# Kernel tuning notes

Hardware: AMD Instinct MI355X
Metric: run time of the kernel (lower is better)

## Reference

```python
import jax, jax.numpy as jnp
import numpy as np

N_NODES = 50000


def _gcn_norm(edge_index, num_nodes):
    # PyG GCNConv default: add self-loops, symmetric normalization D^-1/2 A D^-1/2
    src, dst = edge_index[0], edge_index[1]
    loops = jnp.arange(num_nodes, dtype=src.dtype)
    src = jnp.concatenate([src, loops])
    dst = jnp.concatenate([dst, loops])
    deg = jax.ops.segment_sum(jnp.ones_like(src, dtype=jnp.float32), dst,
                              num_segments=num_nodes)
    dis = jnp.where(deg > 0, jax.lax.rsqrt(jnp.maximum(deg, 1.0)), 0.0)
    norm = dis[src] * dis[dst]  # [E']
    return src, dst, norm


def _gcn_conv(x, W, b, src, dst, norm, num_nodes):
    h = x @ W                                   # [N, out] transform first
    msg = h[src] * norm[:, None]                # [E', out] gather + scale
    agg = jax.ops.segment_sum(msg, dst, num_segments=num_nodes)  # scatter-add
    return agg + b


def setup_inputs() -> dict:
    key = jax.random.key(0)
    k1, k2, k3, k4 = jax.random.split(key, 4)
    n, e, d_in, d_h = N_NODES, 800000, 256, 128
    basic_block = jax.random.normal(k1, (n, d_in), dtype=jnp.float32)
    edge_index = jax.random.randint(k2, (2, e), 0, n, dtype=jnp.int64)
    W1 = jax.random.normal(k3, (d_in, d_h), dtype=jnp.float32) * (1.0 / np.sqrt(d_in))
    b1 = jnp.zeros((d_h,), dtype=jnp.float32)
    W2 = jax.random.normal(k4, (d_h, d_h), dtype=jnp.float32) * (1.0 / np.sqrt(d_h))
    b2 = jnp.zeros((d_h,), dtype=jnp.float32)
    return {"basic_block": basic_block, "edge_index": edge_index,
            "W1": W1, "b1": b1, "W2": W2, "b2": b2}


def reference(basic_block, edge_index, W1, b1, W2, b2):
    n = basic_block.shape[0]
    src, dst, norm = _gcn_norm(edge_index, n)
    x = jax.nn.relu(_gcn_conv(basic_block, W1, b1, src, dst, norm, n))
    x = _gcn_conv(x, W2, b2, src, dst, norm, n)
    return x
```

## Files before the change

### kernel.cpp

```cpp
#include <hip/hip_runtime.h>
#include <hip/hip_bf16.h>
#include <stdint.h>

#define D_H 128

typedef __bf16 bf16_t;
typedef unsigned short u16;
typedef bf16_t bf16x8 __attribute__((ext_vector_type(8)));
typedef bf16_t bf16x4 __attribute__((ext_vector_type(4)));
typedef float  f32x4  __attribute__((ext_vector_type(4)));

__global__ void k_pre(const int* __restrict__ dst, int* __restrict__ cnt4,
                      u16* __restrict__ rank, int E, int Nn, int gcr,
                      const float* __restrict__ W1, bf16_t* __restrict__ W1h,
                      bf16_t* __restrict__ W1l, int K1,
                      const float* __restrict__ W2, bf16_t* __restrict__ W2h,
                      bf16_t* __restrict__ W2l, int K2) {
    int bx = (int)blockIdx.x;
    if (bx < gcr) {
        int e = bx * 256 + threadIdx.x;
        if (e < E) {
            int d = dst[e];
            rank[e] = (u16)atomicAdd(&cnt4[(bx & 3) * Nn + d], 1);
        }
        return;
    }
    int id = (bx - gcr) * 256 + threadIdx.x;
    int n1 = K1 * 128;
    if (id < n1) {
        int k = id >> 7, n = id & 127;
        float w = W1[id];
        bf16_t h = (bf16_t)w;
        W1h[(size_t)n * K1 + k] = h;
        W1l[(size_t)n * K1 + k] = (bf16_t)(w - (float)h);
    } else if (id < n1 + K2 * 128) {
        int id2 = id - n1;
        int k = id2 >> 7, n = id2 & 127;
        float w = W2[id2];
        bf16_t h = (bf16_t)w;
        W2h[(size_t)n * K2 + k] = h;
        W2l[(size_t)n * K2 + k] = (bf16_t)(w - (float)h);
    }
}

__global__ __launch_bounds__(1024) void k_scan1(const int* __restrict__ cnt4,
                                                int* __restrict__ out,
                                                int* __restrict__ bsums,
                                                float* __restrict__ dis, int N) {
    __shared__ int tmp[1024];
    int t = threadIdx.x;
    int i = blockIdx.x * 1024 + t;
    int v = 0;
    if (i < N) {
        v = cnt4[i] + cnt4[N + i] + cnt4[2 * N + i] + cnt4[3 * N + i];
        dis[i] = 1.0f / sqrtf((float)(v + 1));
    }
    tmp[t] = v;
    __syncthreads();
    for (int d = 1; d < 1024; d <<= 1) {
        int x = (t >= d) ? tmp[t - d] : 0;
        __syncthreads();
        tmp[t] += x;
        __syncthreads();
    }
    if (i < N) out[i] = tmp[t] - v;
    if (t == 1023) bsums[blockIdx.x] = tmp[t];
}

__global__ void k_scan2(int* __restrict__ bsums, int nb) {
    __shared__ int tmp[64];
    int t = threadIdx.x;
    int v = (t < nb) ? bsums[t] : 0;
    tmp[t] = v;
    __syncthreads();
    for (int d = 1; d < 64; d <<= 1) {
        int x = (t >= d) ? tmp[t - d] : 0;
        __syncthreads();
        tmp[t] += x;
        __syncthreads();
    }
    if (t < nb) bsums[t] = tmp[t] - v;
}

__global__ __launch_bounds__(1024) void k_scan3(int* __restrict__ off,
                                                const int* __restrict__ bsums,
                                                const int* __restrict__ cnt4,
                                                int* __restrict__ offc,
                                                int N, int E) {
    int i = blockIdx.x * 1024 + threadIdx.x;
    if (i < N) {
        int o = off[i] + bsums[blockIdx.x];
        off[i] = o;
        int c0 = cnt4[i], c1 = cnt4[N + i], c2 = cnt4[2 * N + i];
        offc[i]         = o;
        offc[N + i]     = o + c0;
        offc[2 * N + i] = o + c0 + c1;
        offc[3 * N + i] = o + c0 + c1 + c2;
    }
    if (i == 0) off[N] = E;
}

#define LDK 40
#define FILL_PER 2

__global__ __launch_bounds__(256) void k_mm1fill(
        const float* __restrict__ Af,
        const bf16_t* __restrict__ Wh, const bf16_t* __restrict__ Wl,
        const float* __restrict__ dis, bf16_t* __restrict__ Cb,
        int N, int K,
        const int* __restrict__ src, const int* __restrict__ dst,
        const int* __restrict__ offc, const u16* __restrict__ rank,
        u16* __restrict__ csr16, int E, int totThreads) {
    __shared__ bf16_t AsH[64][LDK];
    __shared__ bf16_t AsL[64][LDK];
    __shared__ bf16_t BsH[64][LDK];
    __shared__ bf16_t BsL[64][LDK];

    const int t    = threadIdx.x;
    const int lane = t & 63;
    const int wave = t >> 6;
    const int row0 = ((int)blockIdx.x >> 1) * 64;
    const int col0 = ((int)blockIdx.x & 1) * 64;
    const int wm   = (wave & 1) * 32;
    const int wn   = (wave >> 1) * 32;
    const int fm   = lane & 15;
    const int fq   = lane >> 4;

    const int g = (int)blockIdx.x * 256 + t;
    int epos[FILL_PER];
    u16 esrc[FILL_PER];
#pragma unroll
    for (int i = 0; i < FILL_PER; i++) {
        int e = g + i * totThreads;
        if (e < E) {
            int d    = dst[e];
            int copy = (e >> 8) & 3;
            epos[i] = offc[copy * N + d] + (int)rank[e];
            esrc[i] = (u16)src[e];
        } else {
            epos[i] = -1;
            esrc[i] = 0;
        }
    }

    f32x4 acc[2][2] = {};

    for (int k0 = 0; k0 < K; k0 += 32) {
        __syncthreads();
#pragma unroll
        for (int i = 0; i < 2; i++) {
            int idx = t + i * 256;
            int r   = idx >> 3;
            int c4  = idx & 7;
            int gr  = row0 + r;
            float4 v = make_float4(0.f, 0.f, 0.f, 0.f);
            if (gr < N) v = *(const float4*)(Af + (size_t)gr * K + k0 + c4 * 4);
            bf16_t h0 = (bf16_t)v.x, h1 = (bf16_t)v.y, h2 = (bf16_t)v.z, h3 = (bf16_t)v.w;
            bf16_t l0 = (bf16_t)(v.x - (float)h0);
            bf16_t l1 = (bf16_t)(v.y - (float)h1);
            bf16_t l2 = (bf16_t)(v.z - (float)h2);
            bf16_t l3 = (bf16_t)(v.w - (float)h3);
            *(bf16x4*)&AsH[r][c4 * 4] = (bf16x4){h0, h1, h2, h3};
            *(bf16x4*)&AsL[r][c4 * 4] = (bf16x4){l0, l1, l2, l3};
        }
        {
            int r  = t >> 2;
            int c8 = t & 3;
            *(bf16x8*)&BsH[r][c8 * 8] = *(const bf16x8*)(Wh + (size_t)(col0 + r) * K + k0 + c8 * 8);
            *(bf16x8*)&BsL[r][c8 * 8] = *(const bf16x8*)(Wl + (size_t)(col0 + r) * K + k0 + c8 * 8);
        }
        __syncthreads();

        bf16x8 ah[2], al[2], bh[2], bl[2];
#pragma unroll
        for (int i = 0; i < 2; i++) {
            ah[i] = *(const bf16x8*)&AsH[wm + i * 16 + fm][fq * 8];
            al[i] = *(const bf16x8*)&AsL[wm + i * 16 + fm][fq * 8];
            bh[i] = *(const bf16x8*)&BsH[wn + i * 16 + fm][fq * 8];
            bl[i] = *(const bf16x8*)&BsL[wn + i * 16 + fm][fq * 8];
        }
#pragma unroll
        for (int mi = 0; mi < 2; mi++)
#pragma unroll
            for (int ni = 0; ni < 2; ni++) {
                acc[mi][ni] = __builtin_amdgcn_mfma_f32_16x16x32_bf16(ah[mi], bh[ni], acc[mi][ni], 0, 0, 0);
                acc[mi][ni] = __builtin_amdgcn_mfma_f32_16x16x32_bf16(ah[mi], bl[ni], acc[mi][ni], 0, 0, 0);
                acc[mi][ni] = __builtin_amdgcn_mfma_f32_16x16x32_bf16(al[mi], bh[ni], acc[mi][ni], 0, 0, 0);
            }
    }

#pragma unroll
    for (int mi = 0; mi < 2; mi++)
#pragma unroll
        for (int r = 0; r < 4; r++) {
            int grow = row0 + wm + mi * 16 + fq * 4 + r;
            if (grow < N) {
                float dr = dis[grow];
#pragma unroll
                for (int ni = 0; ni < 2; ni++)
                    Cb[(size_t)grow * D_H + col0 + wn + ni * 16 + fm] = (bf16_t)(dr * acc[mi][ni][r]);
            }
        }

#pragma unroll
    for (int i = 0; i < FILL_PER; i++)
        if (epos[i] >= 0) csr16[epos[i]] = esrc[i];
}

__global__ __launch_bounds__(256) void k_mm2(const bf16_t* __restrict__ Ah,
                                             const bf16_t* __restrict__ Al,
                                             const bf16_t* __restrict__ Wh,
                                             const bf16_t* __restrict__ Wl,
                                             const float* __restrict__ dis,
                                             bf16_t* __restrict__ Cb,
                                             int N, int K) {
    __shared__ bf16_t AsH[64][LDK];
    __shared__ bf16_t AsL[64][LDK];
    __shared__ bf16_t BsH[64][LDK];
    __shared__ bf16_t BsL[64][LDK];

    const int t    = threadIdx.x;
    const int lane = t & 63;
    const int wave = t >> 6;
    const int row0 = ((int)blockIdx.x >> 1) * 64;
    const int col0 = ((int)blockIdx.x & 1) * 64;
    const int wm   = (wave & 1) * 32;
    const int wn   = (wave >> 1) * 32;
    const int fm   = lane & 15;
    const int fq   = lane >> 4;

    f32x4 acc[2][2] = {};

    for (int k0 = 0; k0 < K; k0 += 32) {
        __syncthreads();
        {
            int r  = t >> 2;
            int c8 = t & 3;
            int gr = row0 + r;
            bf16x8 vh = {}, vl = {};
            if (gr < N) {
                vh = *(const bf16x8*)(Ah + (size_t)gr * K + k0 + c8 * 8);
                vl = *(const bf16x8*)(Al + (size_t)gr * K + k0 + c8 * 8);
            }
            *(bf16x8*)&AsH[r][c8 * 8] = vh;
            *(bf16x8*)&AsL[r][c8 * 8] = vl;
            *(bf16x8*)&BsH[r][c8 * 8] = *(const bf16x8*)(Wh + (size_t)(col0 + r) * K + k0 + c8 * 8);
            *(bf16x8*)&BsL[r][c8 * 8] = *(const bf16x8*)(Wl + (size_t)(col0 + r) * K + k0 + c8 * 8);
        }
        __syncthreads();

        bf16x8 ah[2], al[2], bh[2], bl[2];
#pragma unroll
        for (int i = 0; i < 2; i++) {
            ah[i] = *(const bf16x8*)&AsH[wm + i * 16 + fm][fq * 8];
            al[i] = *(const bf16x8*)&AsL[wm + i * 16 + fm][fq * 8];
            bh[i] = *(const bf16x8*)&BsH[wn + i * 16 + fm][fq * 8];
            bl[i] = *(const bf16x8*)&BsL[wn + i * 16 + fm][fq * 8];
        }
#pragma unroll
        for (int mi = 0; mi < 2; mi++)
#pragma unroll
            for (int ni = 0; ni < 2; ni++) {
                acc[mi][ni] = __builtin_amdgcn_mfma_f32_16x16x32_bf16(ah[mi], bh[ni], acc[mi][ni], 0, 0, 0);
                acc[mi][ni] = __builtin_amdgcn_mfma_f32_16x16x32_bf16(ah[mi], bl[ni], acc[mi][ni], 0, 0, 0);
                acc[mi][ni] = __builtin_amdgcn_mfma_f32_16x16x32_bf16(al[mi], bh[ni], acc[mi][ni], 0, 0, 0);
            }
    }

#pragma unroll
    for (int mi = 0; mi < 2; mi++)
#pragma unroll
        for (int r = 0; r < 4; r++) {
            int grow = row0 + wm + mi * 16 + fq * 4 + r;
            if (grow < N) {
                float dr = dis[grow];
#pragma unroll
                for (int ni = 0; ni < 2; ni++)
                    Cb[(size_t)grow * D_H + col0 + wn + ni * 16 + fm] = (bf16_t)(dr * acc[mi][ni][r]);
            }
        }
}

__global__ __launch_bounds__(256) void k_agg(const bf16_t* __restrict__ Hb,
                                             const float* __restrict__ dis,
                                             const int* __restrict__ off,
                                             const u16* __restrict__ csr16,
                                             const float4* __restrict__ bias4,
                                             float4* __restrict__ outF,
                                             bf16_t* __restrict__ outH,
                                             bf16_t* __restrict__ outL,
                                             int N, int mode) {
    const int slot = threadIdx.x >> 4;
    const int lane = threadIdx.x & 15;
    const int node = blockIdx.x * 16 + slot;
    if (node >= N) return;

    const bf16_t* Hrow = Hb + (size_t)lane * 8;

    float a0[8], a1[8], a2[8], a3[8];
    {
        bf16x8 v = *(const bf16x8*)(Hrow + (size_t)node * D_H);
#pragma unroll
        for (int j = 0; j < 8; j++) { a0[j] = (float)v[j]; a1[j] = 0.f; a2[j] = 0.f; a3[j] = 0.f; }
    }

    int p  = off[node];
    int p1 = off[node + 1];

    for (; p + 4 <= p1; p += 4) {
        int s0 = (int)csr16[p + 0], s1 = (int)csr16[p + 1];
        int s2 = (int)csr16[p + 2], s3 = (int)csr16[p + 3];
        bf16x8 h0 = *(const bf16x8*)(Hrow + (size_t)s0 * D_H);
        bf16x8 h1 = *(const bf16x8*)(Hrow + (size_t)s1 * D_H);
        bf16x8 h2 = *(const bf16x8*)(Hrow + (size_t)s2 * D_H);
        bf16x8 h3 = *(const bf16x8*)(Hrow + (size_t)s3 * D_H);
#pragma unroll
        for (int j = 0; j < 8; j++) {
            a0[j] += (float)h0[j];
            a1[j] += (float)h1[j];
            a2[j] += (float)h2[j];
            a3[j] += (float)h3[j];
        }
    }
    if (p + 2 <= p1) {
        int s0 = (int)csr16[p + 0], s1 = (int)csr16[p + 1];
        bf16x8 h0 = *(const bf16x8*)(Hrow + (size_t)s0 * D_H);
        bf16x8 h1 = *(const bf16x8*)(Hrow + (size_t)s1 * D_H);
#pragma unroll
        for (int j = 0; j < 8; j++) { a0[j] += (float)h0[j]; a1[j] += (float)h1[j]; }
        p += 2;
    }
    if (p < p1) {
        int s0 = (int)csr16[p];
        bf16x8 h0 = *(const bf16x8*)(Hrow + (size_t)s0 * D_H);
#pragma unroll
        for (int j = 0; j < 8; j++) a2[j] += (float)h0[j];
    }

    float sum[8];
#pragma unroll
    for (int j = 0; j < 8; j++) sum[j] = (a0[j] + a1[j]) + (a2[j] + a3[j]);

    const float  di = dis[node];
    const float4 b0 = bias4[lane * 2];
    const float4 b1 = bias4[lane * 2 + 1];
    float v0 = fmaf(di, sum[0], b0.x), v1 = fmaf(di, sum[1], b0.y);
    float v2 = fmaf(di, sum[2], b0.z), v3 = fmaf(di, sum[3], b0.w);
    float v4 = fmaf(di, sum[4], b1.x), v5 = fmaf(di, sum[5], b1.y);
    float v6 = fmaf(di, sum[6], b1.z), v7 = fmaf(di, sum[7], b1.w);

    if (mode == 1) {
        v0 = fmaxf(v0, 0.f); v1 = fmaxf(v1, 0.f); v2 = fmaxf(v2, 0.f); v3 = fmaxf(v3, 0.f);
        v4 = fmaxf(v4, 0.f); v5 = fmaxf(v5, 0.f); v6 = fmaxf(v6, 0.f); v7 = fmaxf(v7, 0.f);
        bf16_t h0 = (bf16_t)v0, h1 = (bf16_t)v1, h2 = (bf16_t)v2, h3 = (bf16_t)v3;
        bf16_t h4 = (bf16_t)v4, h5 = (bf16_t)v5, h6 = (bf16_t)v6, h7 = (bf16_t)v7;
        *(bf16x8*)(outH + (size_t)node * D_H + lane * 8) =
            (bf16x8){h0, h1, h2, h3, h4, h5, h6, h7};
        *(bf16x8*)(outL + (size_t)node * D_H + lane * 8) =
            (bf16x8){(bf16_t)(v0 - (float)h0), (bf16_t)(v1 - (float)h1),
                     (bf16_t)(v2 - (float)h2), (bf16_t)(v3 - (float)h3),
                     (bf16_t)(v4 - (float)h4), (bf16_t)(v5 - (float)h5),
                     (bf16_t)(v6 - (float)h6), (bf16_t)(v7 - (float)h7)};
    } else {
        outF[(size_t)node * 32 + lane * 2]     = make_float4(v0, v1, v2, v3);
        outF[(size_t)node * 32 + lane * 2 + 1] = make_float4(v4, v5, v6, v7);
    }
}

extern "C" void kernel_launch(void* const* d_in, const int* in_sizes, int n_in,
                              void* d_out, int out_size, void* d_ws, size_t ws_size,
                              hipStream_t stream) {
    const float* X  = (const float*)d_in[0];
    const int*   ei = (const int*)d_in[1];
    const float* W1 = (const float*)d_in[2];
    const float* b1 = (const float*)d_in[3];
    const float* W2 = (const float*)d_in[4];
    const float* b2 = (const float*)d_in[5];
    float* out = (float*)d_out;

    const int N  = in_sizes[0] / 256;
    const int E  = in_sizes[1] / 2;
    const int K1 = 256;

    const int* src = ei;
    const int* dst = ei + E;

    uintptr_t p = (uintptr_t)d_ws;
    auto carve = [&](size_t bytes) {
        uintptr_t q = p;
        p += (bytes + 255) & ~(size_t)255;
        return q;
    };
    int*    cnt4  = (int*)carve((size_t)N * 4 * 4);
    int*    off   = (int*)carve((size_t)(N + 1) * 4);
    int*    offc  = (int*)carve((size_t)N * 4 * 4);
    int*    bsums = (int*)carve(64 * 4);
    float*  dis   = (float*)carve((size_t)N * 4);
    u16*    rank  = (u16*)carve((size_t)E * 2);
    u16*    csr16 = (u16*)carve((size_t)E * 2);
    bf16_t* Hb    = (bf16_t*)carve((size_t)N * D_H * 2);
    bf16_t* X1h   = (bf16_t*)carve((size_t)N * D_H * 2);
    bf16_t* X1l   = (bf16_t*)carve((size_t)N * D_H * 2);
    bf16_t* W1h   = (bf16_t*)carve((size_t)K1 * D_H * 2);
    bf16_t* W1l   = (bf16_t*)carve((size_t)K1 * D_H * 2);
    bf16_t* W2h   = (bf16_t*)carve((size_t)D_H * D_H * 2);
    bf16_t* W2l   = (bf16_t*)carve((size_t)D_H * D_H * 2);

    const int nb = (N + 1023) / 1024;

    hipMemsetAsync(cnt4, 0, (size_t)N * 4 * 4, stream);
    const int gcr = (E + 255) / 256;
    const int gw  = (K1 * 128 + D_H * 128 + 255) / 256;
    k_pre<<<gcr + gw, 256, 0, stream>>>(dst, cnt4, rank, E, N, gcr,
                                        W1, W1h, W1l, K1,
                                        W2, W2h, W2l, D_H);
    k_scan1<<<nb, 1024, 0, stream>>>(cnt4, off, bsums, dis, N);
    k_scan2<<<1, 64, 0, stream>>>(bsums, nb);
    k_scan3<<<nb, 1024, 0, stream>>>(off, bsums, cnt4, offc, N, E);

    const int gmm = ((N + 63) / 64) * 2;
    const int gag = (N + 15) / 16;

    k_mm1fill<<<gmm, 256, 0, stream>>>(X, W1h, W1l, dis, Hb, N, K1,
                                       src, dst, offc, rank, csr16, E, gmm * 256);
    k_agg<<<gag, 256, 0, stream>>>(Hb, dis, off, csr16,
                                   (const float4*)b1, nullptr, X1h, X1l, N, 1);

    k_mm2<<<gmm, 256, 0, stream>>>(X1h, X1l, W2h, W2l, dis, Hb, N, D_H);
    k_agg<<<gag, 256, 0, stream>>>(Hb, dis, off, csr16,
                                   (const float4*)b2, (float4*)out, nullptr, nullptr, N, 0);
}
```

Measured before the change: 251.3 us.

## Double-buffer LDS tiles with register prefetch in both GEMM kernels

Both split-bf16 GEMM kernels now use two LDS buffers and prefetch the next K-slices into registers, so global loads overlap with MFMA compute on the current buffer. Each iteration needs one barrier instead of two. K is hardcoded (256 and 128) and the loops are fully unrolled. This doubles LDS use and raises register pressure, which may lower occupancy.

```diff
diff --git a/kernel.cpp b/kernel.cpp
--- a/kernel.cpp
+++ b/kernel.cpp
@@ -111,10 +111,10 @@
         const int* __restrict__ src, const int* __restrict__ dst,
         const int* __restrict__ offc, const u16* __restrict__ rank,
         u16* __restrict__ csr16, int E, int totThreads) {
-    __shared__ bf16_t AsH[64][LDK];
-    __shared__ bf16_t AsL[64][LDK];
-    __shared__ bf16_t BsH[64][LDK];
-    __shared__ bf16_t BsL[64][LDK];
+    __shared__ bf16_t AsH[2][64][LDK];
+    __shared__ bf16_t AsL[2][64][LDK];
+    __shared__ bf16_t BsH[2][64][LDK];
+    __shared__ bf16_t BsL[2][64][LDK];
 
     const int t    = threadIdx.x;
     const int lane = t & 63;
@@ -125,6 +125,11 @@
     const int wn   = (wave >> 1) * 32;
     const int fm   = lane & 15;
     const int fq   = lane >> 4;
+
+    const int arow = t >> 3;
+    const int ac4  = t & 7;
+    const int brow = t >> 2;
+    const int bc8  = t & 3;
 
     const int g = (int)blockIdx.x * 256 + t;
     int epos[FILL_PER];
@@ -145,39 +150,39 @@
 
     f32x4 acc[2][2] = {};
 
-    for (int k0 = 0; k0 < K; k0 += 32) {
-        __syncthreads();
+    auto loadA = [&](float4* va, int k0) {
 #pragma unroll
         for (int i = 0; i < 2; i++) {
-            int idx = t + i * 256;
-            int r   = idx >> 3;
-            int c4  = idx & 7;
-            int gr  = row0 + r;
-            float4 v = make_float4(0.f, 0.f, 0.f, 0.f);
-            if (gr < N) v = *(const float4*)(Af + (size_t)gr * K + k0 + c4 * 4);
+            int gr = row0 + arow + i * 32;
+            va[i] = make_float4(0.f, 0.f, 0.f, 0.f);
+            if (gr < N) va[i] = *(const float4*)(Af + (size_t)gr * 256 + k0 + ac4 * 4);
+        }
+    };
+    auto loadB = [&](bf16x8& vh, bf16x8& vl, int k0) {
+        vh = *(const bf16x8*)(Wh + (size_t)(col0 + brow) * 256 + k0 + bc8 * 8);
+        vl = *(const bf16x8*)(Wl + (size_t)(col0 + brow) * 256 + k0 + bc8 * 8);
+    };
+    auto stage = [&](int b, const float4* va, bf16x8 vh, bf16x8 vl) {
+#pragma unroll
+        for (int i = 0; i < 2; i++) {
+            float4 v = va[i];
             bf16_t h0 = (bf16_t)v.x, h1 = (bf16_t)v.y, h2 = (bf16_t)v.z, h3 = (bf16_t)v.w;
-            bf16_t l0 = (bf16_t)(v.x - (float)h0);
-            bf16_t l1 = (bf16_t)(v.y - (float)h1);
-            bf16_t l2 = (bf16_t)(v.z - (float)h2);
-            bf16_t l3 = (bf16_t)(v.w - (float)h3);
-            *(bf16x4*)&AsH[r][c4 * 4] = (bf16x4){h0, h1, h2, h3};
-            *(bf16x4*)&AsL[r][c4 * 4] = (bf16x4){l0, l1, l2, l3};
-        }
-        {
-            int r  = t >> 2;
-            int c8 = t & 3;
-            *(bf16x8*)&BsH[r][c8 * 8] = *(const bf16x8*)(Wh + (size_t)(col0 + r) * K + k0 + c8 * 8);
-            *(bf16x8*)&BsL[r][c8 * 8] = *(const bf16x8*)(Wl + (size_t)(col0 + r) * K + k0 + c8 * 8);
-        }
-        __syncthreads();
-
+            *(bf16x4*)&AsH[b][arow + i * 32][ac4 * 4] = (bf16x4){h0, h1, h2, h3};
+            *(bf16x4*)&AsL[b][arow + i * 32][ac4 * 4] =
+                (bf16x4){(bf16_t)(v.x - (float)h0), (bf16_t)(v.y - (float)h1),
+                         (bf16_t)(v.z - (float)h2), (bf16_t)(v.w - (float)h3)};
+        }
+        *(bf16x8*)&BsH[b][brow][bc8 * 8] = vh;
+        *(bf16x8*)&BsL[b][brow][bc8 * 8] = vl;
+    };
+    auto compute = [&](int b) {
         bf16x8 ah[2], al[2], bh[2], bl[2];
 #pragma unroll
         for (int i = 0; i < 2; i++) {
-            ah[i] = *(const bf16x8*)&AsH[wm + i * 16 + fm][fq * 8];
-            al[i] = *(const bf16x8*)&AsL[wm + i * 16 + fm][fq * 8];
-            bh[i] = *(const bf16x8*)&BsH[wn + i * 16 + fm][fq * 8];
-            bl[i] = *(const bf16x8*)&BsL[wn + i * 16 + fm][fq * 8];
+            ah[i] = *(const bf16x8*)&AsH[b][wm + i * 16 + fm][fq * 8];
+            al[i] = *(const bf16x8*)&AsL[b][wm + i * 16 + fm][fq * 8];
+            bh[i] = *(const bf16x8*)&BsH[b][wn + i * 16 + fm][fq * 8];
+            bl[i] = *(const bf16x8*)&BsL[b][wn + i * 16 + fm][fq * 8];
         }
 #pragma unroll
         for (int mi = 0; mi < 2; mi++)
@@ -187,6 +192,28 @@
                 acc[mi][ni] = __builtin_amdgcn_mfma_f32_16x16x32_bf16(ah[mi], bl[ni], acc[mi][ni], 0, 0, 0);
                 acc[mi][ni] = __builtin_amdgcn_mfma_f32_16x16x32_bf16(al[mi], bh[ni], acc[mi][ni], 0, 0, 0);
             }
+    };
+
+    float4 vaA[2], vaB[2];
+    bf16x8 vhA, vlA, vhB, vlB;
+    loadA(vaA, 0); loadB(vhA, vlA, 0);
+    stage(0, vaA, vhA, vlA);
+    loadA(vaB, 32); loadB(vhB, vlB, 32);
+    __syncthreads();
+#pragma unroll
+    for (int tt = 0; tt < 8; tt++) {
+        const int cur = tt & 1;
+        if (tt + 1 < 8) {
+            if (cur == 0) {
+                stage(1, vaB, vhB, vlB);
+                if (tt + 2 < 8) { loadA(vaA, (tt + 2) * 32); loadB(vhA, vlA, (tt + 2) * 32); }
+            } else {
+                stage(0, vaA, vhA, vlA);
+                if (tt + 2 < 8) { loadA(vaB, (tt + 2) * 32); loadB(vhB, vlB, (tt + 2) * 32); }
+            }
+        }
+        compute(cur);
+        __syncthreads();
     }
 
 #pragma unroll
@@ -214,10 +241,10 @@
                                              const float* __restrict__ dis,
                                              bf16_t* __restrict__ Cb,
                                              int N, int K) {
-    __shared__ bf16_t AsH[64][LDK];
-    __shared__ bf16_t AsL[64][LDK];
-    __shared__ bf16_t BsH[64][LDK];
-    __shared__ bf16_t BsL[64][LDK];
+    __shared__ bf16_t AsH[2][64][LDK];
+    __shared__ bf16_t AsL[2][64][LDK];
+    __shared__ bf16_t BsH[2][64][LDK];
+    __shared__ bf16_t BsL[2][64][LDK];
 
     const int t    = threadIdx.x;
     const int lane = t & 63;
@@ -229,33 +256,37 @@
     const int fm   = lane & 15;
     const int fq   = lane >> 4;
 
+    const int brow = t >> 2;
+    const int bc8  = t & 3;
+
     f32x4 acc[2][2] = {};
 
-    for (int k0 = 0; k0 < K; k0 += 32) {
-        __syncthreads();
-        {
-            int r  = t >> 2;
-            int c8 = t & 3;
-            int gr = row0 + r;
-            bf16x8 vh = {}, vl = {};
-            if (gr < N) {
-                vh = *(const bf16x8*)(Ah + (size_t)gr * K + k0 + c8 * 8);
-                vl = *(const bf16x8*)(Al + (size_t)gr * K + k0 + c8 * 8);
-            }
-            *(bf16x8*)&AsH[r][c8 * 8] = vh;
-            *(bf16x8*)&AsL[r][c8 * 8] = vl;
-            *(bf16x8*)&BsH[r][c8 * 8] = *(const bf16x8*)(Wh + (size_t)(col0 + r) * K + k0 + c8 * 8);
-            *(bf16x8*)&BsL[r][c8 * 8] = *(const bf16x8*)(Wl + (size_t)(col0 + r) * K + k0 + c8 * 8);
-        }
-        __syncthreads();
-
+    auto loadA = [&](bf16x8& vah, bf16x8& val, int k0) {
+        int gr = row0 + brow;
+        vah = (bf16x8){}; val = (bf16x8){};
+        if (gr < N) {
+            vah = *(const bf16x8*)(Ah + (size_t)gr * 128 + k0 + bc8 * 8);
+            val = *(const bf16x8*)(Al + (size_t)gr * 128 + k0 + bc8 * 8);
+        }
+    };
+    auto loadB = [&](bf16x8& vh, bf16x8& vl, int k0) {
+        vh = *(const bf16x8*)(Wh + (size_t)(col0 + brow) * 128 + k0 + bc8 * 8);
+        vl = *(const bf16x8*)(Wl + (size_t)(col0 + brow) * 128 + k0 + bc8 * 8);
+    };
+    auto stage = [&](int b, bf16x8 vah, bf16x8 val, bf16x8 vbh, bf16x8 vbl) {
+        *(bf16x8*)&AsH[b][brow][bc8 * 8] = vah;
+        *(bf16x8*)&AsL[b][brow][bc8 * 8] = val;
+        *(bf16x8*)&BsH[b][brow][bc8 * 8] = vbh;
+        *(bf16x8*)&BsL[b][brow][bc8 * 8] = vbl;
+    };
+    auto compute = [&](int b) {
         bf16x8 ah[2], al[2], bh[2], bl[2];
 #pragma unroll
         for (int i = 0; i < 2; i++) {
-            ah[i] = *(const bf16x8*)&AsH[wm + i * 16 + fm][fq * 8];
-            al[i] = *(const bf16x8*)&AsL[wm + i * 16 + fm][fq * 8];
-            bh[i] = *(const bf16x8*)&BsH[wn + i * 16 + fm][fq * 8];
-            bl[i] = *(const bf16x8*)&BsL[wn + i * 16 + fm][fq * 8];
+            ah[i] = *(const bf16x8*)&AsH[b][wm + i * 16 + fm][fq * 8];
+            al[i] = *(const bf16x8*)&AsL[b][wm + i * 16 + fm][fq * 8];
+            bh[i] = *(const bf16x8*)&BsH[b][wn + i * 16 + fm][fq * 8];
+            bl[i] = *(const bf16x8*)&BsL[b][wn + i * 16 + fm][fq * 8];
         }
 #pragma unroll
         for (int mi = 0; mi < 2; mi++)
@@ -265,6 +296,27 @@
                 acc[mi][ni] = __builtin_amdgcn_mfma_f32_16x16x32_bf16(ah[mi], bl[ni], acc[mi][ni], 0, 0, 0);
                 acc[mi][ni] = __builtin_amdgcn_mfma_f32_16x16x32_bf16(al[mi], bh[ni], acc[mi][ni], 0, 0, 0);
             }
+    };
+
+    bf16x8 aHA, aLA, bHA, bLA, aHB, aLB, bHB, bLB;
+    loadA(aHA, aLA, 0); loadB(bHA, bLA, 0);
+    stage(0, aHA, aLA, bHA, bLA);
+    loadA(aHB, aLB, 32); loadB(bHB, bLB, 32);
+    __syncthreads();
+#pragma unroll
+    for (int tt = 0; tt < 4; tt++) {
+        const int cur = tt & 1;
+        if (tt + 1 < 4) {
+            if (cur == 0) {
+                stage(1, aHB, aLB, bHB, bLB);
+                if (tt + 2 < 4) { loadA(aHA, aLA, (tt + 2) * 32); loadB(bHA, bLA, (tt + 2) * 32); }
+            } else {
+                stage(0, aHA, aLA, bHA, bLA);
+                if (tt + 2 < 4) { loadA(aHB, aLB, (tt + 2) * 32); loadB(bHB, bLB, (tt + 2) * 32); }
+            }
+        }
+        compute(cur);
+        __syncthreads();
     }
 
 #pragma unroll
```

New measurement: 255.2 us. No clear change (+1.6%).

## Compute full 128-column output per block in both GEMMs with 512 threads

Applied to the files above, without the earlier changes.

Both GEMM kernels now use 512-thread blocks (8 waves) that each cover a 64x128 output tile, instead of two 256-thread blocks each covering 64 columns. The A tile (including the fp32-to-bf16 hi/lo split in the first GEMM) is loaded and converted once per row block rather than twice, which halves A traffic and conversion work. The change hard-codes K strides of 256 and 128 and uses larger B tiles in shared memory. The grid halves and per-block LDS grows, which may reduce occupancy.

```diff
diff --git a/kernel.cpp b/kernel.cpp
--- a/kernel.cpp
+++ b/kernel.cpp
@@ -103,7 +103,7 @@
 #define LDK 40
 #define FILL_PER 2
 
-__global__ __launch_bounds__(256) void k_mm1fill(
+__global__ __launch_bounds__(512) void k_mm1fill(
         const float* __restrict__ Af,
         const bf16_t* __restrict__ Wh, const bf16_t* __restrict__ Wl,
         const float* __restrict__ dis, bf16_t* __restrict__ Cb,
@@ -113,20 +113,24 @@
         u16* __restrict__ csr16, int E, int totThreads) {
     __shared__ bf16_t AsH[64][LDK];
     __shared__ bf16_t AsL[64][LDK];
-    __shared__ bf16_t BsH[64][LDK];
-    __shared__ bf16_t BsL[64][LDK];
+    __shared__ bf16_t BsH[128][LDK];
+    __shared__ bf16_t BsL[128][LDK];
 
     const int t    = threadIdx.x;
     const int lane = t & 63;
     const int wave = t >> 6;
-    const int row0 = ((int)blockIdx.x >> 1) * 64;
-    const int col0 = ((int)blockIdx.x & 1) * 64;
+    const int row0 = (int)blockIdx.x * 64;
     const int wm   = (wave & 1) * 32;
     const int wn   = (wave >> 1) * 32;
     const int fm   = lane & 15;
     const int fq   = lane >> 4;
 
-    const int g = (int)blockIdx.x * 256 + t;
+    const int ar  = t >> 3;
+    const int ac4 = t & 7;
+    const int br  = t >> 2;
+    const int bc8 = t & 3;
+
+    const int g = (int)blockIdx.x * 512 + t;
     int epos[FILL_PER];
     u16 esrc[FILL_PER];
 #pragma unroll
@@ -147,28 +151,18 @@
 
     for (int k0 = 0; k0 < K; k0 += 32) {
         __syncthreads();
-#pragma unroll
-        for (int i = 0; i < 2; i++) {
-            int idx = t + i * 256;
-            int r   = idx >> 3;
-            int c4  = idx & 7;
-            int gr  = row0 + r;
+        {
+            int gr = row0 + ar;
             float4 v = make_float4(0.f, 0.f, 0.f, 0.f);
-            if (gr < N) v = *(const float4*)(Af + (size_t)gr * K + k0 + c4 * 4);
+            if (gr < N) v = *(const float4*)(Af + (size_t)gr * 256 + k0 + ac4 * 4);
             bf16_t h0 = (bf16_t)v.x, h1 = (bf16_t)v.y, h2 = (bf16_t)v.z, h3 = (bf16_t)v.w;
-            bf16_t l0 = (bf16_t)(v.x - (float)h0);
-            bf16_t l1 = (bf16_t)(v.y - (float)h1);
-            bf16_t l2 = (bf16_t)(v.z - (float)h2);
-            bf16_t l3 = (bf16_t)(v.w - (float)h3);
-            *(bf16x4*)&AsH[r][c4 * 4] = (bf16x4){h0, h1, h2, h3};
-            *(bf16x4*)&AsL[r][c4 * 4] = (bf16x4){l0, l1, l2, l3};
-        }
-        {
-            int r  = t >> 2;
-            int c8 = t & 3;
-            *(bf16x8*)&BsH[r][c8 * 8] = *(const bf16x8*)(Wh + (size_t)(col0 + r) * K + k0 + c8 * 8);
-            *(bf16x8*)&BsL[r][c8 * 8] = *(const bf16x8*)(Wl + (size_t)(col0 + r) * K + k0 + c8 * 8);
-        }
+            *(bf16x4*)&AsH[ar][ac4 * 4] = (bf16x4){h0, h1, h2, h3};
+            *(bf16x4*)&AsL[ar][ac4 * 4] =
+                (bf16x4){(bf16_t)(v.x - (float)h0), (bf16_t)(v.y - (float)h1),
+                         (bf16_t)(v.z - (float)h2), (bf16_t)(v.w - (float)h3)};
+        }
+        *(bf16x8*)&BsH[br][bc8 * 8] = *(const bf16x8*)(Wh + (size_t)br * 256 + k0 + bc8 * 8);
+        *(bf16x8*)&BsL[br][bc8 * 8] = *(const bf16x8*)(Wl + (size_t)br * 256 + k0 + bc8 * 8);
         __syncthreads();
 
         bf16x8 ah[2], al[2], bh[2], bl[2];
@@ -198,7 +192,7 @@
                 float dr = dis[grow];
 #pragma unroll
                 for (int ni = 0; ni < 2; ni++)
-                    Cb[(size_t)grow * D_H + col0 + wn + ni * 16 + fm] = (bf16_t)(dr * acc[mi][ni][r]);
+                    Cb[(size_t)grow * D_H + wn + ni * 16 + fm] = (bf16_t)(dr * acc[mi][ni][r]);
             }
         }
 
@@ -207,7 +201,7 @@
         if (epos[i] >= 0) csr16[epos[i]] = esrc[i];
 }
 
-__global__ __launch_bounds__(256) void k_mm2(const bf16_t* __restrict__ Ah,
+__global__ __launch_bounds__(512) void k_mm2(const bf16_t* __restrict__ Ah,
                                              const bf16_t* __restrict__ Al,
                                              const bf16_t* __restrict__ Wh,
                                              const bf16_t* __restrict__ Wl,
@@ -216,37 +210,38 @@
                                              int N, int K) {
     __shared__ bf16_t AsH[64][LDK];
     __shared__ bf16_t AsL[64][LDK];
-    __shared__ bf16_t BsH[64][LDK];
-    __shared__ bf16_t BsL[64][LDK];
+    __shared__ bf16_t BsH[128][LDK];
+    __shared__ bf16_t BsL[128][LDK];
 
     const int t    = threadIdx.x;
     const int lane = t & 63;
     const int wave = t >> 6;
-    const int row0 = ((int)blockIdx.x >> 1) * 64;
-    const int col0 = ((int)blockIdx.x & 1) * 64;
+    const int row0 = (int)blockIdx.x * 64;
     const int wm   = (wave & 1) * 32;
     const int wn   = (wave >> 1) * 32;
     const int fm   = lane & 15;
     const int fq   = lane >> 4;
 
+    const int arow = t >> 3;
+    const int apl  = (t >> 2) & 1;
+    const int ac8  = t & 3;
+    const int br   = t >> 2;
+    const int bc8  = t & 3;
+
     f32x4 acc[2][2] = {};
 
     for (int k0 = 0; k0 < K; k0 += 32) {
         __syncthreads();
         {
-            int r  = t >> 2;
-            int c8 = t & 3;
-            int gr = row0 + r;
-            bf16x8 vh = {}, vl = {};
-            if (gr < N) {
-                vh = *(const bf16x8*)(Ah + (size_t)gr * K + k0 + c8 * 8);
-                vl = *(const bf16x8*)(Al + (size_t)gr * K + k0 + c8 * 8);
-            }
-            *(bf16x8*)&AsH[r][c8 * 8] = vh;
-            *(bf16x8*)&AsL[r][c8 * 8] = vl;
-            *(bf16x8*)&BsH[r][c8 * 8] = *(const bf16x8*)(Wh + (size_t)(col0 + r) * K + k0 + c8 * 8);
-            *(bf16x8*)&BsL[r][c8 * 8] = *(const bf16x8*)(Wl + (size_t)(col0 + r) * K + k0 + c8 * 8);
-        }
+            int gr = row0 + arow;
+            bf16x8 va = {};
+            const bf16_t* Ap = apl ? Al : Ah;
+            if (gr < N) va = *(const bf16x8*)(Ap + (size_t)gr * 128 + k0 + ac8 * 8);
+            if (apl) *(bf16x8*)&AsL[arow][ac8 * 8] = va;
+            else     *(bf16x8*)&AsH[arow][ac8 * 8] = va;
+        }
+        *(bf16x8*)&BsH[br][bc8 * 8] = *(const bf16x8*)(Wh + (size_t)br * 128 + k0 + bc8 * 8);
+        *(bf16x8*)&BsL[br][bc8 * 8] = *(const bf16x8*)(Wl + (size_t)br * 128 + k0 + bc8 * 8);
         __syncthreads();
 
         bf16x8 ah[2], al[2], bh[2], bl[2];
@@ -276,7 +271,7 @@
                 float dr = dis[grow];
 #pragma unroll
                 for (int ni = 0; ni < 2; ni++)
-                    Cb[(size_t)grow * D_H + col0 + wn + ni * 16 + fm] = (bf16_t)(dr * acc[mi][ni][r]);
+                    Cb[(size_t)grow * D_H + wn + ni * 16 + fm] = (bf16_t)(dr * acc[mi][ni][r]);
             }
         }
 }
@@ -418,15 +413,15 @@
     k_scan2<<<1, 64, 0, stream>>>(bsums, nb);
     k_scan3<<<nb, 1024, 0, stream>>>(off, bsums, cnt4, offc, N, E);
 
-    const int gmm = ((N + 63) / 64) * 2;
+    const int gmm = (N + 63) / 64;
     const int gag = (N + 15) / 16;
 
-    k_mm1fill<<<gmm, 256, 0, stream>>>(X, W1h, W1l, dis, Hb, N, K1,
-                                       src, dst, offc, rank, csr16, E, gmm * 256);
+    k_mm1fill<<<gmm, 512, 0, stream>>>(X, W1h, W1l, dis, Hb, N, K1,
+                                       src, dst, offc, rank, csr16, E, gmm * 512);
     k_agg<<<gag, 256, 0, stream>>>(Hb, dis, off, csr16,
                                    (const float4*)b1, nullptr, X1h, X1l, N, 1);
 
-    k_mm2<<<gmm, 256, 0, stream>>>(X1h, X1l, W2h, W2l, dis, Hb, N, D_H);
+    k_mm2<<<gmm, 512, 0, stream>>>(X1h, X1l, W2h, W2l, dis, Hb, N, D_H);
     k_agg<<<gag, 256, 0, stream>>>(Hb, dis, off, csr16,
                                    (const float4*)b2, (float4*)out, nullptr, nullptr, N, 0);
 }
```

Result: no change. 249.9 us (-0.6%).

## Fuse layer-1 aggregation with layer-2 matmul into one kernel

Applied to the files above, without the earlier changes.

Merges the first aggregation kernel and the second GEMM into a single kernel. Each block aggregates 16 nodes, applies bias and ReLU, and stages the hi/lo bf16 split in shared memory. It then multiplies by W2, read straight from global memory, using MFMA. This avoids writing and re-reading the X1h/X1l intermediates (about 25 MB of traffic) and saves one launch. In exchange, each block reloads all of W2 from global/L2, and the MFMA tile is small (16 rows) per block.

```diff
diff --git a/kernel.cpp b/kernel.cpp
--- a/kernel.cpp
+++ b/kernel.cpp
@@ -207,78 +207,125 @@
         if (epos[i] >= 0) csr16[epos[i]] = esrc[i];
 }
 
-__global__ __launch_bounds__(256) void k_mm2(const bf16_t* __restrict__ Ah,
-                                             const bf16_t* __restrict__ Al,
-                                             const bf16_t* __restrict__ Wh,
-                                             const bf16_t* __restrict__ Wl,
-                                             const float* __restrict__ dis,
-                                             bf16_t* __restrict__ Cb,
-                                             int N, int K) {
-    __shared__ bf16_t AsH[64][LDK];
-    __shared__ bf16_t AsL[64][LDK];
-    __shared__ bf16_t BsH[64][LDK];
-    __shared__ bf16_t BsL[64][LDK];
+__global__ __launch_bounds__(256) void k_aggmm(const bf16_t* __restrict__ Hb,
+                                               const float* __restrict__ dis,
+                                               const int* __restrict__ off,
+                                               const u16* __restrict__ csr16,
+                                               const float4* __restrict__ bias4,
+                                               const bf16_t* __restrict__ W2h,
+                                               const bf16_t* __restrict__ W2l,
+                                               bf16_t* __restrict__ Hb2,
+                                               int N) {
+    __shared__ bf16_t XsH[16][136];
+    __shared__ bf16_t XsL[16][136];
 
     const int t    = threadIdx.x;
+    const int slot = t >> 4;
+    const int ln   = t & 15;
+    const int node = blockIdx.x * 16 + slot;
+    const bool live = (node < N);
+
+    const bf16_t* Hrow = Hb + (size_t)ln * 8;
+
+    float a0[8], a1[8], a2[8], a3[8];
+#pragma unroll
+    for (int j = 0; j < 8; j++) { a0[j] = 0.f; a1[j] = 0.f; a2[j] = 0.f; a3[j] = 0.f; }
+    if (live) {
+        bf16x8 v = *(const bf16x8*)(Hrow + (size_t)node * D_H);
+#pragma unroll
+        for (int j = 0; j < 8; j++) a0[j] = (float)v[j];
+    }
+
+    int p  = live ? off[node] : 0;
+    int p1 = live ? off[node + 1] : 0;
+
+    for (; p + 4 <= p1; p += 4) {
+        int s0 = (int)csr16[p + 0], s1 = (int)csr16[p + 1];
+        int s2 = (int)csr16[p + 2], s3 = (int)csr16[p + 3];
+        bf16x8 h0 = *(const bf16x8*)(Hrow + (size_t)s0 * D_H);
+        bf16x8 h1 = *(const bf16x8*)(Hrow + (size_t)s1 * D_H);
+        bf16x8 h2 = *(const bf16x8*)(Hrow + (size_t)s2 * D_H);
+        bf16x8 h3 = *(const bf16x8*)(Hrow + (size_t)s3 * D_H);
+#pragma unroll
+        for (int j = 0; j < 8; j++) {
+            a0[j] += (float)h0[j];
+            a1[j] += (float)h1[j];
+            a2[j] += (float)h2[j];
+            a3[j] += (float)h3[j];
+        }
+    }
+    if (p + 2 <= p1) {
+        int s0 = (int)csr16[p + 0], s1 = (int)csr16[p + 1];
+        bf16x8 h0 = *(const bf16x8*)(Hrow + (size_t)s0 * D_H);
+        bf16x8 h1 = *(const bf16x8*)(Hrow + (size_t)s1 * D_H);
+#pragma unroll
+        for (int j = 0; j < 8; j++) { a0[j] += (float)h0[j]; a1[j] += (float)h1[j]; }
+        p += 2;
+    }
+    if (p < p1) {
+        int s0 = (int)csr16[p];
+        bf16x8 h0 = *(const bf16x8*)(Hrow + (size_t)s0 * D_H);
+#pragma unroll
+        for (int j = 0; j < 8; j++) a2[j] += (float)h0[j];
+    }
+
+    {
+        const float di = live ? dis[node] : 0.f;
+        const float4 b0 = bias4[ln * 2];
+        const float4 b1 = bias4[ln * 2 + 1];
+        float v[8];
+        v[0] = fmaf(di, a0[0] + a1[0] + a2[0] + a3[0], b0.x);
+        v[1] = fmaf(di, a0[1] + a1[1] + a2[1] + a3[1], b0.y);
+        v[2] = fmaf(di, a0[2] + a1[2] + a2[2] + a3[2], b0.z);
+        v[3] = fmaf(di, a0[3] + a1[3] + a2[3] + a3[3], b0.w);
+        v[4] = fmaf(di, a0[4] + a1[4] + a2[4] + a3[4], b1.x);
+        v[5] = fmaf(di, a0[5] + a1[5] + a2[5] + a3[5], b1.y);
+        v[6] = fmaf(di, a0[6] + a1[6] + a2[6] + a3[6], b1.z);
+        v[7] = fmaf(di, a0[7] + a1[7] + a2[7] + a3[7], b1.w);
+        bf16_t hh[8], ll[8];
+#pragma unroll
+        for (int j = 0; j < 8; j++) {
+            float r = fmaxf(v[j], 0.f);
+            hh[j] = (bf16_t)r;
+            ll[j] = (bf16_t)(r - (float)hh[j]);
+        }
+        *(bf16x8*)&XsH[slot][ln * 8] = (bf16x8){hh[0],hh[1],hh[2],hh[3],hh[4],hh[5],hh[6],hh[7]};
+        *(bf16x8*)&XsL[slot][ln * 8] = (bf16x8){ll[0],ll[1],ll[2],ll[3],ll[4],ll[5],ll[6],ll[7]};
+    }
+    __syncthreads();
+
     const int lane = t & 63;
     const int wave = t >> 6;
-    const int row0 = ((int)blockIdx.x >> 1) * 64;
-    const int col0 = ((int)blockIdx.x & 1) * 64;
-    const int wm   = (wave & 1) * 32;
-    const int wn   = (wave >> 1) * 32;
     const int fm   = lane & 15;
     const int fq   = lane >> 4;
-
-    f32x4 acc[2][2] = {};
-
-    for (int k0 = 0; k0 < K; k0 += 32) {
-        __syncthreads();
-        {
-            int r  = t >> 2;
-            int c8 = t & 3;
-            int gr = row0 + r;
-            bf16x8 vh = {}, vl = {};
-            if (gr < N) {
-                vh = *(const bf16x8*)(Ah + (size_t)gr * K + k0 + c8 * 8);
-                vl = *(const bf16x8*)(Al + (size_t)gr * K + k0 + c8 * 8);
-            }
-            *(bf16x8*)&AsH[r][c8 * 8] = vh;
-            *(bf16x8*)&AsL[r][c8 * 8] = vl;
-            *(bf16x8*)&BsH[r][c8 * 8] = *(const bf16x8*)(Wh + (size_t)(col0 + r) * K + k0 + c8 * 8);
-            *(bf16x8*)&BsL[r][c8 * 8] = *(const bf16x8*)(Wl + (size_t)(col0 + r) * K + k0 + c8 * 8);
-        }
-        __syncthreads();
-
-        bf16x8 ah[2], al[2], bh[2], bl[2];
-#pragma unroll
-        for (int i = 0; i < 2; i++) {
-            ah[i] = *(const bf16x8*)&AsH[wm + i * 16 + fm][fq * 8];
-            al[i] = *(const bf16x8*)&AsL[wm + i * 16 + fm][fq * 8];
-            bh[i] = *(const bf16x8*)&BsH[wn + i * 16 + fm][fq * 8];
-            bl[i] = *(const bf16x8*)&BsL[wn + i * 16 + fm][fq * 8];
-        }
-#pragma unroll
-        for (int mi = 0; mi < 2; mi++)
-#pragma unroll
-            for (int ni = 0; ni < 2; ni++) {
-                acc[mi][ni] = __builtin_amdgcn_mfma_f32_16x16x32_bf16(ah[mi], bh[ni], acc[mi][ni], 0, 0, 0);
-                acc[mi][ni] = __builtin_amdgcn_mfma_f32_16x16x32_bf16(ah[mi], bl[ni], acc[mi][ni], 0, 0, 0);
-                acc[mi][ni] = __builtin_amdgcn_mfma_f32_16x16x32_bf16(al[mi], bh[ni], acc[mi][ni], 0, 0, 0);
-            }
-    }
-
-#pragma unroll
-    for (int mi = 0; mi < 2; mi++)
-#pragma unroll
-        for (int r = 0; r < 4; r++) {
-            int grow = row0 + wm + mi * 16 + fq * 4 + r;
-            if (grow < N) {
-                float dr = dis[grow];
-#pragma unroll
-                for (int ni = 0; ni < 2; ni++)
-                    Cb[(size_t)grow * D_H + col0 + wn + ni * 16 + fm] = (bf16_t)(dr * acc[mi][ni][r]);
-            }
-        }
+    const int wn   = wave * 32;
+
+    f32x4 acc[2] = {};
+#pragma unroll
+    for (int ks = 0; ks < 4; ks++) {
+        bf16x8 ah = *(const bf16x8*)&XsH[fm][ks * 32 + fq * 8];
+        bf16x8 al = *(const bf16x8*)&XsL[fm][ks * 32 + fq * 8];
+#pragma unroll
+        for (int ni = 0; ni < 2; ni++) {
+            const size_t boff = (size_t)(wn + ni * 16 + fm) * 128 + ks * 32 + fq * 8;
+            bf16x8 bh = *(const bf16x8*)(W2h + boff);
+            bf16x8 bl = *(const bf16x8*)(W2l + boff);
+            acc[ni] = __builtin_amdgcn_mfma_f32_16x16x32_bf16(ah, bh, acc[ni], 0, 0, 0);
+            acc[ni] = __builtin_amdgcn_mfma_f32_16x16x32_bf16(ah, bl, acc[ni], 0, 0, 0);
+            acc[ni] = __builtin_amdgcn_mfma_f32_16x16x32_bf16(al, bh, acc[ni], 0, 0, 0);
+        }
+    }
+
+#pragma unroll
+    for (int r = 0; r < 4; r++) {
+        int nd = blockIdx.x * 16 + fq * 4 + r;
+        if (nd < N) {
+            float dr = dis[nd];
+#pragma unroll
+            for (int ni = 0; ni < 2; ni++)
+                Hb2[(size_t)nd * D_H + wn + ni * 16 + fm] = (bf16_t)(dr * acc[ni][r]);
+        }
+    }
 }
 
 __global__ __launch_bounds__(256) void k_agg(const bf16_t* __restrict__ Hb,
@@ -287,9 +334,7 @@
                                              const u16* __restrict__ csr16,
                                              const float4* __restrict__ bias4,
                                              float4* __restrict__ outF,
-                                             bf16_t* __restrict__ outH,
-                                             bf16_t* __restrict__ outL,
-                                             int N, int mode) {
+                                             int N) {
     const int slot = threadIdx.x >> 4;
     const int lane = threadIdx.x & 15;
     const int node = blockIdx.x * 16 + slot;
@@ -349,22 +394,8 @@
     float v4 = fmaf(di, sum[4], b1.x), v5 = fmaf(di, sum[5], b1.y);
     float v6 = fmaf(di, sum[6], b1.z), v7 = fmaf(di, sum[7], b1.w);
 
-    if (mode == 1) {
-        v0 = fmaxf(v0, 0.f); v1 = fmaxf(v1, 0.f); v2 = fmaxf(v2, 0.f); v3 = fmaxf(v3, 0.f);
-        v4 = fmaxf(v4, 0.f); v5 = fmaxf(v5, 0.f); v6 = fmaxf(v6, 0.f); v7 = fmaxf(v7, 0.f);
-        bf16_t h0 = (bf16_t)v0, h1 = (bf16_t)v1, h2 = (bf16_t)v2, h3 = (bf16_t)v3;
-        bf16_t h4 = (bf16_t)v4, h5 = (bf16_t)v5, h6 = (bf16_t)v6, h7 = (bf16_t)v7;
-        *(bf16x8*)(outH + (size_t)node * D_H + lane * 8) =
-            (bf16x8){h0, h1, h2, h3, h4, h5, h6, h7};
-        *(bf16x8*)(outL + (size_t)node * D_H + lane * 8) =
-            (bf16x8){(bf16_t)(v0 - (float)h0), (bf16_t)(v1 - (float)h1),
-                     (bf16_t)(v2 - (float)h2), (bf16_t)(v3 - (float)h3),
-                     (bf16_t)(v4 - (float)h4), (bf16_t)(v5 - (float)h5),
-                     (bf16_t)(v6 - (float)h6), (bf16_t)(v7 - (float)h7)};
-    } else {
-        outF[(size_t)node * 32 + lane * 2]     = make_float4(v0, v1, v2, v3);
-        outF[(size_t)node * 32 + lane * 2 + 1] = make_float4(v4, v5, v6, v7);
-    }
+    outF[(size_t)node * 32 + lane * 2]     = make_float4(v0, v1, v2, v3);
+    outF[(size_t)node * 32 + lane * 2 + 1] = make_float4(v4, v5, v6, v7);
 }
 
 extern "C" void kernel_launch(void* const* d_in, const int* in_sizes, int n_in,
@@ -399,8 +430,7 @@
     u16*    rank  = (u16*)carve((size_t)E * 2);
     u16*    csr16 = (u16*)carve((size_t)E * 2);
     bf16_t* Hb    = (bf16_t*)carve((size_t)N * D_H * 2);
-    bf16_t* X1h   = (bf16_t*)carve((size_t)N * D_H * 2);
-    bf16_t* X1l   = (bf16_t*)carve((size_t)N * D_H * 2);
+    bf16_t* Hb2   = (bf16_t*)carve((size_t)N * D_H * 2);
     bf16_t* W1h   = (bf16_t*)carve((size_t)K1 * D_H * 2);
     bf16_t* W1l   = (bf16_t*)carve((size_t)K1 * D_H * 2);
     bf16_t* W2h   = (bf16_t*)carve((size_t)D_H * D_H * 2);
@@ -423,10 +453,8 @@
 
     k_mm1fill<<<gmm, 256, 0, stream>>>(X, W1h, W1l, dis, Hb, N, K1,
                                        src, dst, offc, rank, csr16, E, gmm * 256);
-    k_agg<<<gag, 256, 0, stream>>>(Hb, dis, off, csr16,
-                                   (const float4*)b1, nullptr, X1h, X1l, N, 1);
-
-    k_mm2<<<gmm, 256, 0, stream>>>(X1h, X1l, W2h, W2l, dis, Hb, N, D_H);
-    k_agg<<<gag, 256, 0, stream>>>(Hb, dis, off, csr16,
-                                   (const float4*)b2, (float4*)out, nullptr, nullptr, N, 0);
-}
+    k_aggmm<<<gag, 256, 0, stream>>>(Hb, dis, off, csr16,
+                                     (const float4*)b1, W2h, W2l, Hb2, N);
+    k_agg<<<gag, 256, 0, stream>>>(Hb2, dis, off, csr16,
+                                   (const float4*)b2, (float4*)out, N);
+}
```

Result: no change. 255.8 us (+1.8%).
